# Performance work log

Measured on AMD Instinct MI355X. Metric: run time of the kernel, lower is better.

The kernel has to match this reference:

```python
import jax, jax.numpy as jnp
import numpy as np

N = 50000        # nodes
E = 800000       # edges per meta-path (avg degree 16)
M = 3            # meta-paths
IN = 256         # in_size
HID = 16         # hidden_size (per-head out dim of GATConv)
HEADS = 8
OUT = 8          # out_size (classes)
SA_HID = 128     # StructureAttention hidden_size default
NEG_SLOPE = 0.2  # DGL GATConv leaky_relu default


def setup_inputs() -> dict:
    key = jax.random.key(0)
    ks = jax.random.split(key, 11)
    h = jax.random.normal(ks[0], (N, IN), jnp.float32)
    edges = jax.random.randint(ks[1], (M, 2, E), 0, N, jnp.int32)  # [M, (src,dst), E]
    s = 0.05
    fc_w = jax.random.normal(ks[2], (M, IN, HEADS * HID), jnp.float32) * s
    attn_l = jax.random.normal(ks[3], (M, HEADS, HID), jnp.float32) * s
    attn_r = jax.random.normal(ks[4], (M, HEADS, HID), jnp.float32) * s
    sa_w1 = jax.random.normal(ks[5], (HEADS * HID, SA_HID), jnp.float32) * s
    sa_b1 = jnp.zeros((SA_HID,), jnp.float32)
    sa_w2 = jax.random.normal(ks[6], (SA_HID, 1), jnp.float32) * s
    pred_w = jax.random.normal(ks[7], (HEADS * HID, OUT), jnp.float32) * s
    pred_b = jnp.zeros((OUT,), jnp.float32)
    return {"h": h, "edges": edges, "fc_w": fc_w, "attn_l": attn_l,
            "attn_r": attn_r, "sa_w1": sa_w1, "sa_b1": sa_b1, "sa_w2": sa_w2,
            "pred_w": pred_w, "pred_b": pred_b}


def _gat(h, src, dst, w, al, ar):
    # DGL GATConv, eval mode (dropout=0), activation=elu
    feat = (h @ w).reshape(N, HEADS, HID)                 # [N,H,D]
    el = jnp.einsum('nhd,hd->nh', feat, al)               # [N,H]
    er = jnp.einsum('nhd,hd->nh', feat, ar)               # [N,H]
    e = el[src] + er[dst]                                 # [E,H]
    e = jnp.where(e > 0, e, NEG_SLOPE * e)                # leaky_relu
    # edge softmax over incoming edges of each dst node
    emax = jax.ops.segment_max(e, dst, num_segments=N)    # [N,H]
    ex = jnp.exp(e - emax[dst])                           # [E,H]
    denom = jax.ops.segment_sum(ex, dst, num_segments=N)  # [N,H]
    alpha = ex / denom[dst]                               # [E,H]
    msg = feat[src] * alpha[:, :, None]                   # [E,H,D]
    out = jax.ops.segment_sum(msg, dst, num_segments=N)   # [N,H,D]
    return jax.nn.elu(out).reshape(N, HEADS * HID)        # flatten(1)


def reference(h, edges, fc_w, attn_l, attn_r, sa_w1, sa_b1, sa_w2, pred_w, pred_b):
    # per-meta-path GAT (loop over fixed small set of meta-paths)
    zs = [_gat(h, edges[i, 0], edges[i, 1], fc_w[i], attn_l[i], attn_r[i])
          for i in range(M)]
    z = jnp.stack(zs, axis=1)                             # [N, M, H*D]
    # StructureAttention exactly as in source: softmax over dim 0 (nodes)
    w = jnp.tanh(z @ sa_w1 + sa_b1) @ sa_w2               # [N, M, 1]
    beta = jax.nn.softmax(w, axis=0)                      # softmax over nodes
    fused = (beta * z).sum(0)                             # [M, H*D]
    return fused @ pred_w + pred_b                        # [M, OUT]
```

## Files before the change

kernel.cpp:

```cpp
#include <hip/hip_runtime.h>

#define N_NODES 50000
#define N_EDGES 800000
#define N_META 3
#define IN_DIM 256
#define HD 128
#define HEADS 8
#define HID 16
#define OUT_DIM 8
#define NBKT 196
#define BCAP 5120
#define TILE_E 4096
#define NUMPAD 2064
#define GEMM_BX ((N_NODES + 63) / 64)
#define ELER_BX ((N_NODES * HEADS + 255) / 256)
#define BING_NB (3 * NBKT)

using bf16x8 = __attribute__((ext_vector_type(8))) short;
using f32x4  = __attribute__((ext_vector_type(4))) float;

__device__ __forceinline__ float bf2f(unsigned short u) {
  union { unsigned int i; float f; } x; x.i = ((unsigned int)u) << 16; return x.f;
}
__device__ __forceinline__ unsigned short f2bf(float f) {
  union { float f; unsigned int i; } x; x.f = f;
  unsigned int r = x.i + 0x7fffu + ((x.i >> 16) & 1u);
  return (unsigned short)(r >> 16);
}
__device__ __forceinline__ float tanh_fast(float x) {
  float e = __expf(2.f * x);
  return 1.f - 2.f / (e + 1.f);
}

__global__ __launch_bounds__(256)
void prep_kernel(const float* __restrict__ fcw, const float* __restrict__ w1,
                 unsigned short* __restrict__ fcwT, unsigned short* __restrict__ w1T,
                 float* __restrict__ numpad3, int* __restrict__ gcur) {
  int i = blockIdx.x * 256 + threadIdx.x;
  const int NFC = N_META * IN_DIM * HD;
  const int NW1 = HD * HD;
  const int NNP = N_META * NUMPAD;
  const int NGC = N_META * NBKT;
  if (i < NFC) {
    int p = i / (IN_DIM * HD);
    int rem = i - p * (IN_DIM * HD);
    int k = rem / HD, n = rem - k * HD;
    fcwT[(size_t)p * HD * IN_DIM + n * IN_DIM + k] = f2bf(fcw[i]);
  } else if (i < NFC + NW1) {
    int j = i - NFC;
    int k = j / HD, n = j - k * HD;
    w1T[n * HD + k] = f2bf(w1[j]);
  } else if (i < NFC + NW1 + NNP) {
    numpad3[i - NFC - NW1] = 0.f;
  } else if (i < NFC + NW1 + NNP + NGC) {
    gcur[i - NFC - NW1 - NNP] = 0;
  }
}

__global__ __launch_bounds__(256)
void bin_kernel(const int* __restrict__ edges, int* __restrict__ gcur,
                unsigned int* __restrict__ bktbuf) {
  __shared__ int hist[NBKT];
  __shared__ int gbase[NBKT];
  __shared__ int fill[NBKT];
  int t = threadIdx.x;
  int bx = blockIdx.x;
  int p = bx / NBKT;
  int b = bx - p * NBKT;
  int e0 = b * TILE_E;
  const int* src = edges + (size_t)p * 2 * N_EDGES;
  const int* dst = src + N_EDGES;
  for (int i = t; i < NBKT; i += 256) { hist[i] = 0; fill[i] = 0; }
  __syncthreads();
  for (int i = t; i < TILE_E; i += 256) {
    int e = e0 + i;
    if (e < N_EDGES) atomicAdd(&hist[dst[e] >> 8], 1);
  }
  __syncthreads();
  for (int i = t; i < NBKT; i += 256) {
    int idx = p * NBKT + i;
    gbase[i] = hist[i] ? (idx * BCAP + atomicAdd(&gcur[idx], hist[i])) : 0;
  }
  __syncthreads();
  for (int i = t; i < TILE_E; i += 256) {
    int e = e0 + i;
    if (e < N_EDGES) {
      int d = dst[e];
      int b2 = d >> 8;
      int r = atomicAdd(&fill[b2], 1);
      bktbuf[gbase[b2] + r] = ((unsigned int)(d & 255) << 16) | (unsigned int)src[e];
    }
  }
}

__global__ __launch_bounds__(256)
void gemm_kernel(const float* __restrict__ A,
                 const unsigned short* __restrict__ BT,
                 unsigned short* __restrict__ Cb, int nrows) {
  __shared__ unsigned short As[64 * 40];
  __shared__ unsigned short Bs[384 * 40];
  int t = threadIdx.x;
  int w = t >> 6, l = t & 63, q = l >> 4, s = l & 15;
  int row0 = blockIdx.x * 64;
  f32x4 acc[4][6] = {};
  for (int k0 = 0; k0 < IN_DIM; k0 += 32) {
    {
      int r = t >> 2, c = (t & 3) * 8;
      int gr = row0 + r;
      float4 a0, a1;
      if (gr < nrows) {
        a0 = *(const float4*)(A + (size_t)gr * IN_DIM + k0 + c);
        a1 = *(const float4*)(A + (size_t)gr * IN_DIM + k0 + c + 4);
      } else {
        a0 = make_float4(0.f, 0.f, 0.f, 0.f); a1 = a0;
      }
      ushort4 u0, u1;
      u0.x = f2bf(a0.x); u0.y = f2bf(a0.y); u0.z = f2bf(a0.z); u0.w = f2bf(a0.w);
      u1.x = f2bf(a1.x); u1.y = f2bf(a1.y); u1.z = f2bf(a1.z); u1.w = f2bf(a1.w);
      *(ushort4*)&As[r * 40 + c]     = u0;
      *(ushort4*)&As[r * 40 + c + 4] = u1;
    }
    {
      int n = t >> 1, c = (t & 1) * 16;
      #pragma unroll
      for (int mm = 0; mm < 3; ++mm) {
        const unsigned short* BTm =
            BT + (size_t)mm * HD * IN_DIM + (size_t)n * IN_DIM + k0 + c;
        uint4 b0 = *(const uint4*)(BTm);
        uint4 b1 = *(const uint4*)(BTm + 8);
        unsigned short* Bsm = Bs + (mm * 128 + n) * 40 + c;
        *(uint4*)&Bsm[0] = b0;
        *(uint4*)&Bsm[8] = b1;
      }
    }
    __syncthreads();
    bf16x8 bfv[6];
    #pragma unroll
    for (int nt = 0; nt < 6; ++nt)
      bfv[nt] = *(bf16x8*)&Bs[(w * 96 + nt * 16 + s) * 40 + q * 8];
    #pragma unroll
    for (int mt = 0; mt < 4; ++mt) {
      bf16x8 af = *(bf16x8*)&As[(mt * 16 + s) * 40 + q * 8];
      #pragma unroll
      for (int nt = 0; nt < 6; ++nt)
        acc[mt][nt] = __builtin_amdgcn_mfma_f32_16x16x32_bf16(af, bfv[nt], acc[mt][nt], 0, 0, 0);
    }
    __syncthreads();
  }
  #pragma unroll
  for (int mt = 0; mt < 4; ++mt) {
    #pragma unroll
    for (int nt = 0; nt < 6; ++nt) {
      int gc = w * 96 + nt * 16 + s;
      int mm = gc >> 7, cim = gc & 127;
      unsigned short* Cm = Cb + (size_t)mm * N_NODES * HD;
      #pragma unroll
      for (int r = 0; r < 4; ++r) {
        int gr = row0 + mt * 16 + q * 4 + r;
        if (gr < nrows) Cm[(size_t)gr * HD + cim] = f2bf(acc[mt][nt][r]);
      }
    }
  }
}

__global__ __launch_bounds__(256)
void sort_eler_kernel(const int* __restrict__ gcur,
                      const unsigned int* __restrict__ bktbuf,
                      int* __restrict__ offsB, int* __restrict__ offsE,
                      int* __restrict__ csr,
                      const unsigned short* __restrict__ featb3,
                      const float* __restrict__ al, const float* __restrict__ ar,
                      float* __restrict__ el3, float* __restrict__ er3) {
  __shared__ int lh[256];
  __shared__ int cur[256];
  __shared__ int wsum[4];
  int p = blockIdx.y;
  int t = threadIdx.x;
  if (blockIdx.x < NBKT) {
    int b = blockIdx.x;
    int lane = t & 63, wid = t >> 6;
    int idx = p * NBKT + b;
    int S = idx * BCAP;
    int E = S + gcur[idx];
    int node0 = b * 256;
    int nn = min(256, N_NODES - node0);
    int gi0 = p * N_NODES + node0;
    lh[t] = 0;
    __syncthreads();
    for (int i = S + t; i < E; i += 256) atomicAdd(&lh[bktbuf[i] >> 16], 1);
    __syncthreads();
    int v = lh[t];
    int s = v;
    #pragma unroll
    for (int d = 1; d < 64; d <<= 1) {
      int x = __shfl_up(s, d);
      if (lane >= d) s += x;
    }
    if (lane == 63) wsum[wid] = s;
    __syncthreads();
    int woff = 0;
    #pragma unroll
    for (int k = 0; k < 4; ++k) if (k < wid) woff += wsum[k];
    int excl = S + woff + s - v;
    if (t < nn) {
      offsB[gi0 + t] = excl;
      offsE[gi0 + t] = excl + v;
    }
    cur[t] = excl;
    __syncthreads();
    for (int i = S + t; i < E; i += 256) {
      unsigned int rec = bktbuf[i];
      int pos = atomicAdd(&cur[rec >> 16], 1);
      csr[pos] = (int)(rec & 0xffffu);
    }
  } else {
    int i = (blockIdx.x - NBKT) * 256 + t;
    if (i >= N_NODES * HEADS) return;
    int node = i >> 3, hh = i & 7;
    const unsigned short* f =
        featb3 + (size_t)p * N_NODES * HD + (size_t)node * HD + hh * HID;
    uint4 u0 = *(const uint4*)(f);
    uint4 u1 = *(const uint4*)(f + 8);
    unsigned int uu[8] = {u0.x, u0.y, u0.z, u0.w, u1.x, u1.y, u1.z, u1.w};
    const float* alm = al + p * HD + hh * HID;
    const float* arm = ar + p * HD + hh * HID;
    float sl = 0.f, sr = 0.f;
    #pragma unroll
    for (int q = 0; q < 8; ++q) {
      float v0 = __uint_as_float(uu[q] << 16);
      float v1 = __uint_as_float(uu[q] & 0xffff0000u);
      int d = q * 2;
      sl += v0 * alm[d] + v1 * alm[d + 1];
      sr += v0 * arm[d] + v1 * arm[d + 1];
    }
    el3[(size_t)p * N_NODES * HEADS + i] = sl;
    er3[(size_t)p * N_NODES * HEADS + i] = sr;
  }
}

__global__ __launch_bounds__(256)
void aggregate_kernel(const int* __restrict__ offsB3, const int* __restrict__ offsE3,
                      const int* __restrict__ csr,
                      const uint4* __restrict__ featb3_u4,
                      const float* __restrict__ el3, const float* __restrict__ er3,
                      uint4* __restrict__ zb3_u4, int m) {
  int node = blockIdx.x * 4 + (threadIdx.x >> 6);
  if (node >= N_NODES) return;
  const uint4* featb_u4 = featb3_u4 + (size_t)m * N_NODES * 16;
  const float* el = el3 + (size_t)m * N_NODES * HEADS;
  const float* er = er3 + (size_t)m * N_NODES * HEADS;
  uint4* z_u4 = zb3_u4 + (size_t)m * N_NODES * 16;
  int lane = threadIdx.x & 63;
  int qg = lane >> 4;
  int li = lane & 15;
  int ch = li >> 1;
  int beg = offsB3[m * N_NODES + node], end = offsE3[m * N_NODES + node];
  float erh = er[node * HEADS + ch];
  float ssum = 0.f;
  float a[8] = {};
  for (int i = beg; i < end; i += 16) {
    int nk = end - i;
    int last = end - 1;
    int s0 = csr[min(i + qg,      last)];
    int s1 = csr[min(i + qg + 4,  last)];
    int s2 = csr[min(i + qg + 8,  last)];
    int s3 = csr[min(i + qg + 12, last)];
    uint4 v0 = featb_u4[(size_t)s0 * 16 + li];
    uint4 v1 = featb_u4[(size_t)s1 * 16 + li];
    uint4 v2 = featb_u4[(size_t)s2 * 16 + li];
    uint4 v3 = featb_u4[(size_t)s3 * 16 + li];
    float e0 = el[s0 * HEADS + ch] + erh;
    float e1 = el[s1 * HEADS + ch] + erh;
    float e2 = el[s2 * HEADS + ch] + erh;
    float e3 = el[s3 * HEADS + ch] + erh;
    e0 = e0 > 0.f ? e0 : 0.2f * e0;
    e1 = e1 > 0.f ? e1 : 0.2f * e1;
    e2 = e2 > 0.f ? e2 : 0.2f * e2;
    e3 = e3 > 0.f ? e3 : 0.2f * e3;
    float w0 = (qg      < nk) ? __expf(e0) : 0.f;
    float w1 = (qg + 4  < nk) ? __expf(e1) : 0.f;
    float w2 = (qg + 8  < nk) ? __expf(e2) : 0.f;
    float w3 = (qg + 12 < nk) ? __expf(e3) : 0.f;
    ssum += (w0 + w1) + (w2 + w3);
    a[0] += w0 * __uint_as_float(v0.x << 16);
    a[1] += w0 * __uint_as_float(v0.x & 0xffff0000u);
    a[2] += w0 * __uint_as_float(v0.y << 16);
    a[3] += w0 * __uint_as_float(v0.y & 0xffff0000u);
    a[4] += w0 * __uint_as_float(v0.z << 16);
    a[5] += w0 * __uint_as_float(v0.z & 0xffff0000u);
    a[6] += w0 * __uint_as_float(v0.w << 16);
    a[7] += w0 * __uint_as_float(v0.w & 0xffff0000u);
    a[0] += w1 * __uint_as_float(v1.x << 16);
    a[1] += w1 * __uint_as_float(v1.x & 0xffff0000u);
    a[2] += w1 * __uint_as_float(v1.y << 16);
    a[3] += w1 * __uint_as_float(v1.y & 0xffff0000u);
    a[4] += w1 * __uint_as_float(v1.z << 16);
    a[5] += w1 * __uint_as_float(v1.z & 0xffff0000u);
    a[6] += w1 * __uint_as_float(v1.w << 16);
    a[7] += w1 * __uint_as_float(v1.w & 0xffff0000u);
    a[0] += w2 * __uint_as_float(v2.x << 16);
    a[1] += w2 * __uint_as_float(v2.x & 0xffff0000u);
    a[2] += w2 * __uint_as_float(v2.y << 16);
    a[3] += w2 * __uint_as_float(v2.y & 0xffff0000u);
    a[4] += w2 * __uint_as_float(v2.z << 16);
    a[5] += w2 * __uint_as_float(v2.z & 0xffff0000u);
    a[6] += w2 * __uint_as_float(v2.w << 16);
    a[7] += w2 * __uint_as_float(v2.w & 0xffff0000u);
    a[0] += w3 * __uint_as_float(v3.x << 16);
    a[1] += w3 * __uint_as_float(v3.x & 0xffff0000u);
    a[2] += w3 * __uint_as_float(v3.y << 16);
    a[3] += w3 * __uint_as_float(v3.y & 0xffff0000u);
    a[4] += w3 * __uint_as_float(v3.z << 16);
    a[5] += w3 * __uint_as_float(v3.z & 0xffff0000u);
    a[6] += w3 * __uint_as_float(v3.w << 16);
    a[7] += w3 * __uint_as_float(v3.w & 0xffff0000u);
  }
  #pragma unroll
  for (int j = 0; j < 8; ++j) {
    a[j] += __shfl_xor(a[j], 16);
    a[j] += __shfl_xor(a[j], 32);
  }
  ssum += __shfl_xor(ssum, 16);
  ssum += __shfl_xor(ssum, 32);
  float inv = (end > beg) ? 1.f / ssum : 0.f;
  if (qg == 0) {
    #pragma unroll
    for (int j = 0; j < 8; ++j) {
      float z = a[j] * inv;
      a[j] = z > 0.f ? z : __expf(z) - 1.f;
    }
    uint4 o;
    unsigned int p0, p1, p2, p3;
    asm("v_cvt_pk_bf16_f32 %0, %1, %2" : "=v"(p0) : "v"(a[0]), "v"(a[1]));
    asm("v_cvt_pk_bf16_f32 %0, %1, %2" : "=v"(p1) : "v"(a[2]), "v"(a[3]));
    asm("v_cvt_pk_bf16_f32 %0, %1, %2" : "=v"(p2) : "v"(a[4]), "v"(a[5]));
    asm("v_cvt_pk_bf16_f32 %0, %1, %2" : "=v"(p3) : "v"(a[6]), "v"(a[7]));
    o.x = p0; o.y = p1; o.z = p2; o.w = p3;
    z_u4[(size_t)node * 16 + li] = o;
  }
}

__global__ __launch_bounds__(256)
void w_gemm_mfma(const unsigned short* __restrict__ Zb3,
                 const unsigned short* __restrict__ BT,
                 const float* __restrict__ B1, const float* __restrict__ W2,
                 float* __restrict__ numpad3, int nrows) {
  __shared__ unsigned short Bs[128 * 136];
  __shared__ unsigned short As[64 * 136];
  __shared__ float wrow[64];
  __shared__ float part[4][64][2];
  __shared__ float dpart[4];
  int tid = threadIdx.x;
  int m = blockIdx.y;
  const unsigned short* Zb = Zb3 + (size_t)m * N_NODES * HD;
  float* numpad = numpad3 + (size_t)m * NUMPAD;
  int w = tid >> 6, l = tid & 63, q = l >> 4, s = l & 15;
  {
    int n = tid >> 1, c0 = (tid & 1) * 64;
    #pragma unroll
    for (int j = 0; j < 8; ++j)
      *(uint4*)&Bs[n * 136 + c0 + j * 8] = *(const uint4*)(BT + n * HD + c0 + j * 8);
  }
  float b1v[8], w2v[8];
  #pragma unroll
  for (int f = 0; f < 8; ++f) { b1v[f] = B1[f * 16 + s]; w2v[f] = W2[f * 16 + s]; }
  float a0 = 0.f, a1 = 0.f, ld = 0.f;
  for (int t = 0; t < 4; ++t) {
    int row0 = blockIdx.x * 256 + t * 64;
    __syncthreads();
    {
      int r = tid >> 2, c0 = (tid & 3) * 32;
      int gr = row0 + r;
      if (gr < nrows) {
        #pragma unroll
        for (int j = 0; j < 4; ++j)
          *(uint4*)&As[r * 136 + c0 + j * 8] =
              *(const uint4*)(Zb + (size_t)gr * HD + c0 + j * 8);
      } else {
        uint4 z = make_uint4(0, 0, 0, 0);
        #pragma unroll
        for (int j = 0; j < 4; ++j) *(uint4*)&As[r * 136 + c0 + j * 8] = z;
      }
    }
    __syncthreads();
    f32x4 acc[8] = {};
    #pragma unroll
    for (int kc = 0; kc < 4; ++kc) {
      bf16x8 af = *(bf16x8*)&As[(w * 16 + s) * 136 + kc * 32 + q * 8];
      #pragma unroll
      for (int f = 0; f < 8; ++f) {
        bf16x8 bf = *(bf16x8*)&Bs[(f * 16 + s) * 136 + kc * 32 + q * 8];
        acc[f] = __builtin_amdgcn_mfma_f32_16x16x32_bf16(af, bf, acc[f], 0, 0, 0);
      }
    }
    #pragma unroll
    for (int r = 0; r < 4; ++r) {
      float p = 0.f;
      #pragma unroll
      for (int f = 0; f < 8; ++f) p += tanh_fast(acc[f][r] + b1v[f]) * w2v[f];
      p += __shfl_xor(p, 1); p += __shfl_xor(p, 2);
      p += __shfl_xor(p, 4); p += __shfl_xor(p, 8);
      if (s == 0) wrow[w * 16 + q * 4 + r] = p;
    }
    __syncthreads();
    for (int r = w; r < 64; r += 4) {
      int gr = row0 + r;
      if (gr < nrows) {
        float e = __expf(wrow[r]);
        unsigned int v = *(const unsigned int*)&As[r * 136 + 2 * l];
        a0 += e * __uint_as_float(v << 16);
        a1 += e * __uint_as_float(v & 0xffff0000u);
        if (l == 0) ld += e;
      }
    }
  }
  part[w][l][0] = a0;
  part[w][l][1] = a1;
  if (l == 0) dpart[w] = ld;
  __syncthreads();
  if (w == 0) {
    float s0 = part[0][l][0] + part[1][l][0] + part[2][l][0] + part[3][l][0];
    float s1 = part[0][l][1] + part[1][l][1] + part[2][l][1] + part[3][l][1];
    atomicAdd(&numpad[(2 * l) * 16], s0);
    atomicAdd(&numpad[(2 * l + 1) * 16], s1);
    if (l == 0)
      atomicAdd(&numpad[128 * 16], dpart[0] + dpart[1] + dpart[2] + dpart[3]);
  }
}

__global__ void final_kernel(const float* __restrict__ numpad,
                             const float* __restrict__ PW, const float* __restrict__ PB,
                             float* __restrict__ out) {
  int t = threadIdx.x;
  if (t >= N_META * OUT_DIM) return;
  int m = t >> 3, o = t & 7;
  const float* np = numpad + m * NUMPAD;
  float inv = 1.0f / np[128 * 16];
  float s = 0.f;
  for (int k = 0; k < HD; ++k) s += np[k * 16] * PW[k * OUT_DIM + o];
  out[t] = s * inv + PB[o];
}

extern "C" void kernel_launch(void* const* d_in, const int* in_sizes, int n_in,
                              void* d_out, int out_size, void* d_ws, size_t ws_size,
                              hipStream_t stream) {
  (void)in_sizes; (void)n_in; (void)out_size; (void)ws_size;
  const float* h     = (const float*)d_in[0];
  const int*   edges = (const int*)d_in[1];
  const float* fcw   = (const float*)d_in[2];
  const float* al    = (const float*)d_in[3];
  const float* ar    = (const float*)d_in[4];
  const float* w1    = (const float*)d_in[5];
  const float* b1    = (const float*)d_in[6];
  const float* w2    = (const float*)d_in[7];
  const float* pw    = (const float*)d_in[8];
  const float* pb    = (const float*)d_in[9];
  float* out = (float*)d_out;

  char* ws = (char*)d_ws;
  size_t off = 0;
  auto alloc = [&](size_t bytes) -> void* {
    void* p = ws + off;
    off = (off + bytes + 255) & ~(size_t)255;
    return p;
  };
  unsigned short* featb3 = (unsigned short*)alloc((size_t)N_META * N_NODES * HD * 2);
  unsigned short* zb3    = (unsigned short*)alloc((size_t)N_META * N_NODES * HD * 2);
  unsigned short* fcwT   = (unsigned short*)alloc((size_t)N_META * HD * IN_DIM * 2);
  unsigned short* w1T    = (unsigned short*)alloc((size_t)HD * HD * 2);
  float* el3 = (float*)alloc((size_t)N_META * N_NODES * HEADS * 4);
  float* er3 = (float*)alloc((size_t)N_META * N_NODES * HEADS * 4);
  int* gcur  = (int*)alloc((size_t)N_META * NBKT * 4);
  int* offsB = (int*)alloc((size_t)N_META * N_NODES * 4);
  int* offsE = (int*)alloc((size_t)N_META * N_NODES * 4);
  unsigned int* bktbuf = (unsigned int*)alloc((size_t)N_META * NBKT * BCAP * 4);
  int* csr   = (int*)alloc((size_t)N_META * NBKT * BCAP * 4);
  float* numpad = (float*)alloc((size_t)N_META * NUMPAD * 4);

  const int PREP_N = N_META * IN_DIM * HD + HD * HD + N_META * NUMPAD + N_META * NBKT;
  prep_kernel<<<(PREP_N + 255) / 256, 256, 0, stream>>>(
      fcw, w1, fcwT, w1T, numpad, gcur);

  bin_kernel<<<BING_NB, 256, 0, stream>>>(edges, gcur, bktbuf);
  gemm_kernel<<<GEMM_BX, 256, 0, stream>>>(h, fcwT, featb3, N_NODES);

  dim3 bgrid_(NBKT + ELER_BX, N_META);
  sort_eler_kernel<<<bgrid_, 256, 0, stream>>>(
      gcur, bktbuf, offsB, offsE, csr, featb3, al, ar, el3, er3);

  for (int mm = 0; mm < N_META; ++mm) {
    aggregate_kernel<<<(N_NODES + 3) / 4, 256, 0, stream>>>(
        offsB, offsE, csr, (const uint4*)featb3, el3, er3, (uint4*)zb3, mm);
  }

  dim3 wgrid((N_NODES + 255) / 256, N_META);
  w_gemm_mfma<<<wgrid, 256, 0, stream>>>(zb3, w1T, b1, w2, numpad, N_NODES);

  final_kernel<<<1, 64, 0, stream>>>(numpad, pw, pb, out);
}
```

Before: 363.0 us.

## Restructure structure-attention GEMM: one 64-row tile per block, direct A-fragment loads

The w_gemm_mfma kernel now processes one 64-row tile per block instead of looping over four, which launches four times as many blocks. A fragments are loaded straight from global memory into registers instead of being staged in LDS. The B matrix uses an XOR-swizzled LDS layout in place of padding, and the exp weights are computed once per row, with the denominator reduced by wave shuffles. The aim is to raise occupancy and parallelism and to cut LDS traffic and barriers. The cost is that the B tile is reloaded into LDS by four times as many blocks, and there are more atomic adds into numpad.

```diff
diff --git a/kernel.cpp b/kernel.cpp
--- a/kernel.cpp
+++ b/kernel.cpp
@@ -345,86 +345,79 @@
                  const unsigned short* __restrict__ BT,
                  const float* __restrict__ B1, const float* __restrict__ W2,
                  float* __restrict__ numpad3, int nrows) {
-  __shared__ unsigned short Bs[128 * 136];
-  __shared__ unsigned short As[64 * 136];
-  __shared__ float wrow[64];
+  __shared__ unsigned short Bs[128 * 128];
+  __shared__ float ew[64];
   __shared__ float part[4][64][2];
-  __shared__ float dpart[4];
   int tid = threadIdx.x;
   int m = blockIdx.y;
   const unsigned short* Zb = Zb3 + (size_t)m * N_NODES * HD;
   float* numpad = numpad3 + (size_t)m * NUMPAD;
   int w = tid >> 6, l = tid & 63, q = l >> 4, s = l & 15;
+  int row0 = blockIdx.x * 64;
   {
-    int n = tid >> 1, c0 = (tid & 1) * 64;
-    #pragma unroll
-    for (int j = 0; j < 8; ++j)
-      *(uint4*)&Bs[n * 136 + c0 + j * 8] = *(const uint4*)(BT + n * HD + c0 + j * 8);
+    int n = tid >> 1;
+    int jb = (tid & 1) * 8;
+    #pragma unroll
+    for (int jj = 0; jj < 8; ++jj) {
+      int j = jb + jj;
+      *(uint4*)&Bs[n * 128 + ((j ^ (n & 15)) << 3)] =
+          *(const uint4*)(BT + n * HD + j * 8);
+    }
   }
   float b1v[8], w2v[8];
   #pragma unroll
   for (int f = 0; f < 8; ++f) { b1v[f] = B1[f * 16 + s]; w2v[f] = W2[f * 16 + s]; }
-  float a0 = 0.f, a1 = 0.f, ld = 0.f;
-  for (int t = 0; t < 4; ++t) {
-    int row0 = blockIdx.x * 256 + t * 64;
-    __syncthreads();
-    {
-      int r = tid >> 2, c0 = (tid & 3) * 32;
-      int gr = row0 + r;
-      if (gr < nrows) {
-        #pragma unroll
-        for (int j = 0; j < 4; ++j)
-          *(uint4*)&As[r * 136 + c0 + j * 8] =
-              *(const uint4*)(Zb + (size_t)gr * HD + c0 + j * 8);
-      } else {
-        uint4 z = make_uint4(0, 0, 0, 0);
-        #pragma unroll
-        for (int j = 0; j < 4; ++j) *(uint4*)&As[r * 136 + c0 + j * 8] = z;
-      }
-    }
-    __syncthreads();
-    f32x4 acc[8] = {};
-    #pragma unroll
-    for (int kc = 0; kc < 4; ++kc) {
-      bf16x8 af = *(bf16x8*)&As[(w * 16 + s) * 136 + kc * 32 + q * 8];
-      #pragma unroll
-      for (int f = 0; f < 8; ++f) {
-        bf16x8 bf = *(bf16x8*)&Bs[(f * 16 + s) * 136 + kc * 32 + q * 8];
-        acc[f] = __builtin_amdgcn_mfma_f32_16x16x32_bf16(af, bf, acc[f], 0, 0, 0);
-      }
-    }
-    #pragma unroll
-    for (int r = 0; r < 4; ++r) {
-      float p = 0.f;
-      #pragma unroll
-      for (int f = 0; f < 8; ++f) p += tanh_fast(acc[f][r] + b1v[f]) * w2v[f];
-      p += __shfl_xor(p, 1); p += __shfl_xor(p, 2);
-      p += __shfl_xor(p, 4); p += __shfl_xor(p, 8);
-      if (s == 0) wrow[w * 16 + q * 4 + r] = p;
-    }
-    __syncthreads();
-    for (int r = w; r < 64; r += 4) {
-      int gr = row0 + r;
-      if (gr < nrows) {
-        float e = __expf(wrow[r]);
-        unsigned int v = *(const unsigned int*)&As[r * 136 + 2 * l];
-        a0 += e * __uint_as_float(v << 16);
-        a1 += e * __uint_as_float(v & 0xffff0000u);
-        if (l == 0) ld += e;
-      }
-    }
+  int gra = min(row0 + w * 16 + s, nrows - 1);
+  const unsigned short* arow = Zb + (size_t)gra * HD;
+  bf16x8 af[4];
+  #pragma unroll
+  for (int kc = 0; kc < 4; ++kc)
+    af[kc] = *(const bf16x8*)(arow + kc * 32 + q * 8);
+  __syncthreads();
+  f32x4 acc[8] = {};
+  #pragma unroll
+  for (int kc = 0; kc < 4; ++kc) {
+    #pragma unroll
+    for (int f = 0; f < 8; ++f) {
+      bf16x8 bf = *(bf16x8*)&Bs[(f * 16 + s) * 128 + ((((kc << 2) | q) ^ s) << 3)];
+      acc[f] = __builtin_amdgcn_mfma_f32_16x16x32_bf16(af[kc], bf, acc[f], 0, 0, 0);
+    }
+  }
+  #pragma unroll
+  for (int r = 0; r < 4; ++r) {
+    float p = 0.f;
+    #pragma unroll
+    for (int f = 0; f < 8; ++f) p += tanh_fast(acc[f][r] + b1v[f]) * w2v[f];
+    p += __shfl_xor(p, 1); p += __shfl_xor(p, 2);
+    p += __shfl_xor(p, 4); p += __shfl_xor(p, 8);
+    if (s == 0) {
+      int rr = w * 16 + q * 4 + r;
+      ew[rr] = (row0 + rr < nrows) ? __expf(p) : 0.f;
+    }
+  }
+  __syncthreads();
+  const unsigned int* Zu = (const unsigned int*)Zb;
+  int rmax = min(64, nrows - row0);
+  float a0 = 0.f, a1 = 0.f;
+  for (int r = w; r < rmax; r += 4) {
+    float e = ew[r];
+    unsigned int v = Zu[(size_t)(row0 + r) * 64 + l];
+    a0 += e * __uint_as_float(v << 16);
+    a1 += e * __uint_as_float(v & 0xffff0000u);
   }
   part[w][l][0] = a0;
   part[w][l][1] = a1;
-  if (l == 0) dpart[w] = ld;
   __syncthreads();
   if (w == 0) {
     float s0 = part[0][l][0] + part[1][l][0] + part[2][l][0] + part[3][l][0];
     float s1 = part[0][l][1] + part[1][l][1] + part[2][l][1] + part[3][l][1];
     atomicAdd(&numpad[(2 * l) * 16], s0);
     atomicAdd(&numpad[(2 * l + 1) * 16], s1);
-    if (l == 0)
-      atomicAdd(&numpad[128 * 16], dpart[0] + dpart[1] + dpart[2] + dpart[3]);
+    float ldv = ew[l];
+    ldv += __shfl_xor(ldv, 1);  ldv += __shfl_xor(ldv, 2);
+    ldv += __shfl_xor(ldv, 4);  ldv += __shfl_xor(ldv, 8);
+    ldv += __shfl_xor(ldv, 16); ldv += __shfl_xor(ldv, 32);
+    if (l == 0) atomicAdd(&numpad[128 * 16], ldv);
   }
 }
 
@@ -493,7 +486,7 @@
         offsB, offsE, csr, (const uint4*)featb3, el3, er3, (uint4*)zb3, mm);
   }
 
-  dim3 wgrid((N_NODES + 255) / 256, N_META);
+  dim3 wgrid((N_NODES + 63) / 64, N_META);
   w_gemm_mfma<<<wgrid, 256, 0, stream>>>(zb3, w1T, b1, w2, numpad, N_NODES);
 
   final_kernel<<<1, 64, 0, stream>>>(numpad, pw, pb, out);
```

New measurement: 369.4 us. Within noise of the previous version (+1.8%).
